# Performance work log

Measured on AMD Instinct MI355X. Metric: run time of the kernel, lower is better.

The kernel has to match this reference:

```python
import jax, jax.numpy as jnp
import numpy as np

B, N, P, L = 32, 4096, 256, 16
DR = 128           # rel_dim = args.rgcn_hidden_size
H = 128            # rnn_hidden_size (unidirectional -> rnn_opt_dim == H)
D = H
NUM_REL = 400      # num_rels * 2


def setup_inputs() -> dict:
    key = jax.random.key(0)
    ks = jax.random.split(key, 12)
    s = 0.05
    graph_embed = jax.random.normal(ks[0], (B, N, DR), jnp.float32)
    node_opt = jax.random.normal(ks[1], (B, D), jnp.float32)
    node_idx = jax.random.randint(ks[2], (B, P, L), 0, N)
    rel_idx = jax.random.randint(ks[3], (B, P, L), 0, NUM_REL)
    path_lens = jax.random.randint(ks[4], (B, P), 1, L + 1)  # in [1, L]
    rel_embeds = jax.random.normal(ks[5], (NUM_REL, DR), jnp.float32) * s
    W_ih = jax.random.normal(ks[6], (4 * H, 2 * DR), jnp.float32) * s
    W_hh = jax.random.normal(ks[7], (4 * H, H), jnp.float32) * s
    b_ih = jnp.zeros((4 * H,), jnp.float32)
    b_hh = jnp.zeros((4 * H,), jnp.float32)
    in_proj_w = jax.random.normal(ks[8], (3 * D, D), jnp.float32) * s
    in_proj_b = jnp.zeros((3 * D,), jnp.float32)
    out_proj_w = jax.random.normal(ks[9], (D, D), jnp.float32) * s
    out_proj_b = jnp.zeros((D,), jnp.float32)
    return dict(graph_embed=graph_embed, node_opt=node_opt, rel_embeds=rel_embeds,
                W_ih=W_ih, W_hh=W_hh, b_ih=b_ih, b_hh=b_hh,
                in_proj_w=in_proj_w, in_proj_b=in_proj_b,
                out_proj_w=out_proj_w, out_proj_b=out_proj_b,
                node_idx=node_idx, rel_idx=rel_idx, path_lens=path_lens)


def _forward(graph_embed, node_opt, rel_embeds, W_ih, W_hh, b_ih, b_hh,
             in_proj_w, in_proj_b, out_proj_w, out_proj_b,
             node_idx, rel_idx, path_lens):
    b, n, dr = graph_embed.shape
    p, l = node_idx.shape[1], node_idx.shape[2]
    h = W_hh.shape[1]
    dt = graph_embed.dtype

    t = jnp.arange(l)
    # node embedding valid for steps < len; rel valid for steps < len-1 ('Padr' at last step -> zero rel half)
    node_mask = (t[None, None, :] < path_lens[:, :, None]).astype(dt)[..., None]
    rel_mask = (t[None, None, :] < (path_lens - 1)[:, :, None]).astype(dt)[..., None]

    batch_ix = jnp.arange(b)[:, None, None]
    node_e = graph_embed[batch_ix, node_idx]            # [B,P,L,DR]
    rel_e = rel_embeds[rel_idx]                          # [B,P,L,DR]
    x = jnp.concatenate([node_e * node_mask, rel_e * rel_mask], axis=-1)
    x = x.reshape(b * p, l, 2 * dr)                      # packed path sequences

    bias = b_ih + b_hh

    def step(carry, xt):
        hh, cc = carry
        g = xt @ W_ih.T + hh @ W_hh.T + bias
        i, f, gg, o = jnp.split(g, 4, axis=-1)
        i = jax.nn.sigmoid(i); f = jax.nn.sigmoid(f)
        gg = jnp.tanh(gg); o = jax.nn.sigmoid(o)
        cc = f * cc + i * gg
        hh = o * jnp.tanh(cc)
        return (hh, cc), hh

    h0 = jnp.zeros((b * p, h), dt)
    _, ys = jax.lax.scan(step, (h0, h0), jnp.swapaxes(x, 0, 1))
    ys = jnp.swapaxes(ys, 0, 1).reshape(b, p, l, h)

    # last valid LSTM output per path (== pack_padded_sequence semantics, unidirectional)
    idx = jnp.broadcast_to((path_lens - 1)[:, :, None, None], (b, p, 1, h))
    last = jnp.take_along_axis(ys, idx, axis=2).squeeze(2)   # [B,P,H]

    # single-head MultiheadAttention: query = node_opt, keys/values = path encodings
    Wq, Wk, Wv = jnp.split(in_proj_w, 3, axis=0)
    bq, bk, bv = jnp.split(in_proj_b, 3)
    q = node_opt @ Wq.T + bq                                  # [B,D]
    k = last @ Wk.T + bk                                      # [B,P,D]
    v = last @ Wv.T + bv
    scale = 1.0 / jnp.sqrt(jnp.asarray(q.shape[-1], dt))
    attn = jax.nn.softmax(jnp.einsum('bd,bpd->bp', q, k) * scale, axis=-1)
    ctx = jnp.einsum('bp,bpd->bd', attn, v)
    return ctx @ out_proj_w.T + out_proj_b                    # [B,D]


def reference(graph_embed, node_opt, rel_embeds, W_ih, W_hh, b_ih, b_hh,
              in_proj_w, in_proj_b, out_proj_w, out_proj_b,
              node_idx, rel_idx, path_lens):
    return _forward(graph_embed, node_opt, rel_embeds, W_ih, W_hh, b_ih, b_hh,
                    in_proj_w, in_proj_b, out_proj_w, out_proj_b,
                    node_idx, rel_idx, path_lens)
```

## Files before the change

### kernel.cpp

```cpp
#include <hip/hip_runtime.h>
#include <hip/hip_bf16.h>


#define B_    32
#define N_    4096
#define L_    16
#define DR_   128
#define H_    128
#define G4_   512
#define AST2  264
#define NPATH 8192
#define NPB   32

typedef unsigned short bfraw;
typedef short short8 __attribute__((ext_vector_type(8)));
typedef float f32x4 __attribute__((ext_vector_type(4)));

__device__ int   g_isbf16;
__device__ int   g_isi64;
__device__ __align__(16) bfraw g_Wcat[G4_ * 256];
__device__ __align__(16) float g_relproj[400 * G4_];
__device__ float g_bias[G4_];
__device__ int   g_perm[NPATH];
__device__ float g_last[NPATH * H_];

#define BAR() asm volatile("s_waitcnt lgkmcnt(0)\n\ts_barrier" ::: "memory")

__device__ __forceinline__ float bfc(bfraw v) {
    return __uint_as_float(((unsigned)v) << 16);
}
__device__ __forceinline__ bfraw f2b(float f) {
    unsigned u = __float_as_uint(f);
    return (bfraw)((u + 0x7FFFu + ((u >> 16) & 1u)) >> 16);
}
__device__ __forceinline__ unsigned pk2(float a, float b) {
    return (unsigned)f2b(a) | ((unsigned)f2b(b) << 16);
}
__device__ __forceinline__ float ld(const void* p, size_t i, int isbf) {
    return isbf ? bfc(((const bfraw*)p)[i]) : ((const float*)p)[i];
}
__device__ __forceinline__ float sigf(float x) {
    return __builtin_amdgcn_rcpf(1.0f + __expf(-x));
}
__device__ __forceinline__ float tanhfast(float x) {
    return 2.0f * sigf(2.0f * x) - 1.0f;
}

__device__ __forceinline__ float dot128(const float* __restrict__ w,
                                        const float* __restrict__ s) {
    float acc = 0.f;
    #pragma unroll
    for (int i = 0; i < 32; ++i) {
        const float4 wv = *(const float4*)(w + i * 4);
        acc = fmaf(wv.x, s[i*4+0], fmaf(wv.y, s[i*4+1],
              fmaf(wv.z, s[i*4+2], fmaf(wv.w, s[i*4+3], acc))));
    }
    return acc;
}

__global__ __launch_bounds__(512) void k_prep(
    const void* __restrict__ node_opt, const int* __restrict__ node_idx,
    const void* __restrict__ rel_embeds,
    const void* __restrict__ W_ih, const void* __restrict__ W_hh,
    const void* __restrict__ b_ih, const void* __restrict__ b_hh,
    const int* __restrict__ path_lens)
{
    __shared__ float relv[DR_];
    __shared__ int s_big, s_nz, hist[16], cur[16];
    const int tid = threadIdx.x;
    const int blk = blockIdx.x;

    if (tid == 0) { s_big = 0; s_nz = 0; }
    __syncthreads();
    {
        const unsigned short* u = (const unsigned short*)node_opt;
        int big = 0;
        #pragma unroll
        for (int i = 0; i < 4; ++i) {
            const float v = fabsf(bfc(u[tid + i * 512]));
            big |= !(v < 1.0e3f);
        }
        if (big) s_big = 1;
        if (node_idx[2 * tid + 1] != 0) s_nz = 1;
    }
    __syncthreads();
    const int isbf = s_big ? 0 : 1;
    const int i64  = s_nz ? 0 : 1;

    if (blk < 400) {
        const int r = blk;
        if (tid < DR_) relv[tid] = ld(rel_embeds, (size_t)r * DR_ + tid, isbf);
        __syncthreads();
        const int n = tid;
        float s;
        if (isbf) {
            s = 0.f;
            for (int d = 0; d < DR_; ++d)
                s = fmaf(relv[d], bfc(((const bfraw*)W_ih)[(size_t)n * 256 + 128 + d]), s);
        } else {
            s = dot128((const float*)W_ih + (size_t)n * 256 + 128, relv);
        }
        g_relproj[r * G4_ + ((n & 127) << 2) + (n >> 7)] = s;
    } else if (blk < 656) {
        const int idx = (blk - 400) * 512 + tid;
        const int n = idx >> 8, k = idx & 255;
        const float v = (k < H_) ? ld(W_hh, (size_t)n * H_ + k, isbf)
                                 : ld(W_ih, (size_t)n * 256 + (k - H_), isbf);
        g_Wcat[n * 256 + k] = f2b(v);
    } else {
        if (tid == 0) { g_isbf16 = isbf; g_isi64 = i64; }
        g_bias[tid] = ld(b_ih, tid, isbf) + ld(b_hh, tid, isbf);
        if (tid < 16) hist[tid] = 0;
        __syncthreads();
        for (int p = tid; p < NPATH; p += 512) {
            const int len = i64 ? path_lens[2 * p] : path_lens[p];
            atomicAdd(&hist[len - 1], 1);
        }
        __syncthreads();
        if (tid == 0) {
            int off = 0;
            for (int b = 15; b >= 0; --b) { cur[b] = off; off += hist[b]; }
        }
        __syncthreads();
        for (int p = tid; p < NPATH; p += 512) {
            const int len = i64 ? path_lens[2 * p] : path_lens[p];
            const int pos = atomicAdd(&cur[len - 1], 1);
            g_perm[pos] = p;
        }
    }
}

__global__ __launch_bounds__(512, 2) void k_lstm(
    const void* __restrict__ graph_embed,
    const int*  __restrict__ node_idx,
    const int*  __restrict__ rel_idx,
    const int*  __restrict__ path_lens)
{
    __shared__ __align__(16) bfraw A[NPB][AST2];
    __shared__ int s_pid[NPB], s_len[NPB];
    __shared__ int s_nid[NPB][L_], s_rid[NPB][L_];

    const int isbf = g_isbf16;
    const int i64  = g_isi64;
    const int tid  = threadIdx.x;

    if (tid < NPB) {
        const int pid = g_perm[blockIdx.x * NPB + tid];
        s_pid[tid] = pid;
        s_len[tid] = i64 ? path_lens[2 * pid] : path_lens[pid];
    }
    __syncthreads();
    {
        const int m = tid >> 4, t = tid & 15;
        const int idx = s_pid[m] * L_ + t;
        s_nid[m][t] = i64 ? node_idx[2 * idx] : node_idx[idx];
        s_rid[m][t] = i64 ? rel_idx[2 * idx]  : rel_idx[idx];
    }
    {
        const int m = tid >> 4, i0 = (tid & 15) * 8;
        *(uint4*)&A[m][i0] = make_uint4(0, 0, 0, 0);
    }
    __syncthreads();

    int maxlen = 0;
    #pragma unroll
    for (int m = 0; m < NPB; ++m) maxlen = max(maxlen, s_len[m]);

    const int w    = tid >> 6;
    const int l    = tid & 63;
    const int quad = l >> 4;
    const int col  = l & 15;
    const int u0   = w * 16 + col;

    short8 wreg[8][4];
    float bq4[4];
    #pragma unroll
    for (int g = 0; g < 4; ++g) {
        bq4[g] = g_bias[g * 128 + u0];
        const bfraw* wrow = g_Wcat + (size_t)(g * 128 + u0) * 256 + quad * 8;
        #pragma unroll
        for (int ck = 0; ck < 8; ++ck)
            wreg[ck][g] = *(const short8*)(wrow + ck * 32);
    }

    const int pm  = tid >> 4;
    const int pi0 = (tid & 15) * 8;
    const size_t gbase = (size_t)(s_pid[pm] >> 8) * (size_t)(N_ * DR_);

    {
        const int nid = s_nid[pm][0];
        uint4 npk;
        if (isbf) {
            npk = *(const uint4*)((const bfraw*)graph_embed + gbase + (size_t)nid * DR_ + pi0);
        } else {
            const float* gp = (const float*)graph_embed + gbase + (size_t)nid * DR_ + pi0;
            const uint4 q0 = *(const uint4*)gp;
            const uint4 q1 = *(const uint4*)(gp + 4);
            const float* a = (const float*)&q0;
            const float* b = (const float*)&q1;
            npk = make_uint4(pk2(a[0],a[1]), pk2(a[2],a[3]),
                             pk2(b[0],b[1]), pk2(b[2],b[3]));
        }
        *(uint4*)&A[pm][128 + pi0] = npk;
    }
    __syncthreads();

    float c[2][4];
    #pragma unroll
    for (int mt = 0; mt < 2; ++mt)
        #pragma unroll
        for (int r = 0; r < 4; ++r) c[mt][r] = 0.f;

    uint4 pn0, pn1;

    for (int t = 0; t < maxlen; ++t) {
        if (t + 1 < maxlen) {
            const int nid = s_nid[pm][t + 1];
            if (isbf) {
                pn0 = *(const uint4*)((const bfraw*)graph_embed + gbase + (size_t)nid * DR_ + pi0);
            } else {
                const float* gp = (const float*)graph_embed + gbase + (size_t)nid * DR_ + pi0;
                pn0 = *(const uint4*)gp; pn1 = *(const uint4*)(gp + 4);
            }
        }

        f32x4 acc[2][4];
        #pragma unroll
        for (int mt = 0; mt < 2; ++mt)
            #pragma unroll
            for (int g = 0; g < 4; ++g) {
                const float b = bq4[g];
                acc[mt][g][0] = b; acc[mt][g][1] = b;
                acc[mt][g][2] = b; acc[mt][g][3] = b;
            }
        #pragma unroll
        for (int ck = 0; ck < 8; ++ck) {
            const short8 a0 = *(const short8*)&A[col][ck * 32 + quad * 8];
            const short8 a1 = *(const short8*)&A[16 + col][ck * 32 + quad * 8];
            #pragma unroll
            for (int g = 0; g < 4; ++g) {
                acc[0][g] = __builtin_amdgcn_mfma_f32_16x16x32_bf16(a0, wreg[ck][g], acc[0][g], 0, 0, 0);
                acc[1][g] = __builtin_amdgcn_mfma_f32_16x16x32_bf16(a1, wreg[ck][g], acc[1][g], 0, 0, 0);
            }
        }
        __builtin_amdgcn_sched_barrier(0);

        f32x4 rlv[2][4];
        #pragma unroll
        for (int mt = 0; mt < 2; ++mt)
            #pragma unroll
            for (int r = 0; r < 4; ++r) {
                const int m = mt * 16 + quad * 4 + r;
                rlv[mt][r] = *(const f32x4*)(g_relproj + (size_t)s_rid[m][t] * G4_ + u0 * 4);
            }

        float hv[2][4];
        #pragma unroll
        for (int mt = 0; mt < 2; ++mt)
            #pragma unroll
            for (int r = 0; r < 4; ++r) {
                const int m = mt * 16 + quad * 4 + r;
                const float relm = (t < s_len[m] - 1) ? 1.0f : 0.0f;
                const float ig = sigf(acc[mt][0][r] + relm * rlv[mt][r][0]);
                const float fg = sigf(acc[mt][1][r] + relm * rlv[mt][r][1]);
                const float gg = tanhfast(acc[mt][2][r] + relm * rlv[mt][r][2]);
                const float og = sigf(acc[mt][3][r] + relm * rlv[mt][r][3]);
                const float cc = fg * c[mt][r] + ig * gg;
                c[mt][r] = cc;
                hv[mt][r] = og * tanhfast(cc);
            }

        BAR();

        #pragma unroll
        for (int mt = 0; mt < 2; ++mt)
            #pragma unroll
            for (int r = 0; r < 4; ++r) {
                const int m = mt * 16 + quad * 4 + r;
                A[m][u0] = f2b(hv[mt][r]);
                if (t == s_len[m] - 1)
                    g_last[(size_t)s_pid[m] * H_ + u0] = hv[mt][r];
            }

        if (t + 1 < maxlen) {
            uint4 npk = make_uint4(0, 0, 0, 0);
            if (t + 1 < s_len[pm]) {
                if (isbf) npk = pn0;
                else {
                    const float* a = (const float*)&pn0;
                    const float* b = (const float*)&pn1;
                    npk = make_uint4(pk2(a[0],a[1]), pk2(a[2],a[3]),
                                     pk2(b[0],b[1]), pk2(b[2],b[3]));
                }
            }
            *(uint4*)&A[pm][128 + pi0] = npk;
        }

        BAR();
    }
}

__global__ __launch_bounds__(256) void k_attn(
    const void* __restrict__ node_opt,
    const void* __restrict__ in_proj_w,
    const void* __restrict__ in_proj_b,
    const void* __restrict__ out_proj_w,
    const void* __restrict__ out_proj_b,
    float* __restrict__ out)
{
    const int isbf = g_isbf16;
    const int b = blockIdx.x, tid = threadIdx.x;
    __shared__ __align__(16) float s_no[128], q[128], qk[128], sv2[2][128], ctx[128];
    __shared__ float logits[256];
    __shared__ float red[12];

    if (tid < 128) s_no[tid] = ld(node_opt, b * 128 + tid, isbf);
    __syncthreads();
    if (tid < 128) {
        float s;
        if (isbf) {
            s = 0.f;
            for (int j = 0; j < 128; ++j)
                s = fmaf(s_no[j], ld(in_proj_w, (size_t)tid * 128 + j, 1), s);
        } else {
            s = dot128((const float*)in_proj_w + (size_t)tid * 128, s_no);
        }
        q[tid] = s + ld(in_proj_b, tid, isbf);
    }
    __syncthreads();
    if (tid < 128) {
        float s = 0.f;
        for (int j = 0; j < 128; ++j)
            s = fmaf(q[j], ld(in_proj_w, (size_t)(128 + j) * 128 + tid, isbf), s);
        qk[tid] = s;
    } else if (tid == 128) {
        float s = 0.f;
        for (int j = 0; j < 128; ++j)
            s = fmaf(q[j], ld(in_proj_b, 128 + j, isbf), s);
        red[10] = s;
    }
    __syncthreads();
    {
        const float* lp = g_last + ((size_t)b * 256 + tid) * H_;
        const float s = dot128(lp, qk);
        logits[tid] = (s + red[10]) * 0.08838834764831845f;
    }
    __syncthreads();
    float v = logits[tid];
    #pragma unroll
    for (int off = 32; off > 0; off >>= 1) v = fmaxf(v, __shfl_xor(v, off, 64));
    if ((tid & 63) == 0) red[tid >> 6] = v;
    __syncthreads();
    if (tid == 0) red[8] = fmaxf(fmaxf(red[0], red[1]), fmaxf(red[2], red[3]));
    __syncthreads();
    const float e = __expf(logits[tid] - red[8]);
    float sum = e;
    #pragma unroll
    for (int off = 32; off > 0; off >>= 1) sum += __shfl_xor(sum, off, 64);
    if ((tid & 63) == 0) red[4 + (tid >> 6)] = sum;
    __syncthreads();
    if (tid == 0) red[9] = red[4] + red[5] + red[6] + red[7];
    __syncthreads();
    logits[tid] = e / red[9];
    __syncthreads();
    {
        const int u = tid & 127, half = tid >> 7;
        float s = 0.f;
        const float* lb = g_last + ((size_t)b * 256 + half * 128) * H_ + u;
        for (int p = 0; p < 128; ++p)
            s = fmaf(logits[half * 128 + p], lb[(size_t)p * H_], s);
        sv2[half][u] = s;
    }
    __syncthreads();
    if (tid < 128) q[tid] = sv2[0][tid] + sv2[1][tid];
    __syncthreads();
    if (tid < 128) {
        float s;
        if (isbf) {
            s = 0.f;
            for (int u = 0; u < 128; ++u)
                s = fmaf(q[u], ld(in_proj_w, (size_t)(256 + tid) * 128 + u, 1), s);
        } else {
            s = dot128((const float*)in_proj_w + (size_t)(256 + tid) * 128, q);
        }
        ctx[tid] = s + ld(in_proj_b, 256 + tid, isbf);
    }
    __syncthreads();
    if (tid < 128) {
        float s;
        if (isbf) {
            s = 0.f;
            for (int d = 0; d < 128; ++d)
                s = fmaf(ctx[d], ld(out_proj_w, (size_t)tid * 128 + d, 1), s);
        } else {
            s = dot128((const float*)out_proj_w + (size_t)tid * 128, ctx);
        }
        out[b * 128 + tid] = s + ld(out_proj_b, tid, isbf);
    }
}

extern "C" void kernel_launch(void* const* d_in, const int* in_sizes, int n_in,
                              void* d_out, int out_size, void* d_ws, size_t ws_size,
                              hipStream_t stream)
{
    const void* graph_embed = d_in[0];
    const void* node_opt    = d_in[1];
    const void* rel_embeds  = d_in[2];
    const void* W_ih        = d_in[3];
    const void* W_hh        = d_in[4];
    const void* b_ih        = d_in[5];
    const void* b_hh        = d_in[6];
    const void* in_proj_w   = d_in[7];
    const void* in_proj_b   = d_in[8];
    const void* out_proj_w  = d_in[9];
    const void* out_proj_b  = d_in[10];
    const int* node_idx  = (const int*)d_in[11];
    const int* rel_idx   = (const int*)d_in[12];
    const int* path_lens = (const int*)d_in[13];
    (void)d_ws; (void)ws_size; (void)in_sizes; (void)n_in; (void)out_size;

    hipLaunchKernelGGL(k_prep, dim3(657), dim3(512), 0, stream,
                       node_opt, node_idx, rel_embeds, W_ih, W_hh, b_ih, b_hh,
                       path_lens);
    hipLaunchKernelGGL(k_lstm, dim3(NPATH / NPB), dim3(512), 0, stream,
                       graph_embed, node_idx, rel_idx, path_lens);
    hipLaunchKernelGGL(k_attn, dim3(B_), dim3(256), 0, stream,
                       node_opt, in_proj_w, in_proj_b, out_proj_w, out_proj_b,
                       (float*)d_out);
}
```

Baseline: 219.4 us.

## Software-pipeline LSTM step across two path halves to overlap MFMA with gates

```diff
diff --git a/kernel.cpp b/kernel.cpp
--- a/kernel.cpp
+++ b/kernel.cpp
@@ -130,6 +130,80 @@
     }
 }
 
+
+#define DO_MFMA(ACC, BASE)                                                    \
+    {                                                                         \
+        _Pragma("unroll")                                                     \
+        for (int g = 0; g < 4; ++g) {                                         \
+            const float bb_ = bq4[g];                                         \
+            ACC[g][0] = bb_; ACC[g][1] = bb_; ACC[g][2] = bb_; ACC[g][3] = bb_; \
+        }                                                                     \
+        _Pragma("unroll")                                                     \
+        for (int ck = 0; ck < 8; ++ck) {                                      \
+            const short8 av_ = *(const short8*)&A[(BASE) + col][ck * 32 + quad * 8]; \
+            _Pragma("unroll")                                                 \
+            for (int g = 0; g < 4; ++g)                                       \
+                ACC[g] = __builtin_amdgcn_mfma_f32_16x16x32_bf16(             \
+                    av_, wreg[ck][g], ACC[g], 0, 0, 0);                       \
+        }                                                                     \
+    }
+
+#define RL_ADDR(RLO, MBASE, T)                                                \
+    {                                                                         \
+        _Pragma("unroll")                                                     \
+        for (int r = 0; r < 4; ++r)                                           \
+            RLO[r] = s_rid[(MBASE) + quad * 4 + r][T] * (G4_ * 4) + u0 * 16;  \
+    }
+
+#define DO_GATES(ACC, MT, MBASE, T, RLO)                                      \
+    {                                                                         \
+        f32x4 rlv_[4];                                                        \
+        _Pragma("unroll")                                                     \
+        for (int r = 0; r < 4; ++r)                                           \
+            rlv_[r] = *(const f32x4*)((const char*)g_relproj + RLO[r]);       \
+        _Pragma("unroll")                                                     \
+        for (int r = 0; r < 4; ++r) {                                         \
+            const int m_ = (MBASE) + quad * 4 + r;                            \
+            const float relm_ = ((T) < s_len[m_] - 1) ? 1.0f : 0.0f;          \
+            const float ig_ = sigf(ACC[0][r] + relm_ * rlv_[r][0]);           \
+            const float fg_ = sigf(ACC[1][r] + relm_ * rlv_[r][1]);           \
+            const float gg_ = tanhfast(ACC[2][r] + relm_ * rlv_[r][2]);       \
+            const float og_ = sigf(ACC[3][r] + relm_ * rlv_[r][3]);           \
+            const float cc_ = fg_ * c[MT][r] + ig_ * gg_;                     \
+            c[MT][r] = cc_;                                                   \
+            const float hh_ = og_ * tanhfast(cc_);                           \
+            A[m_][u0] = f2b(hh_);                                             \
+            if ((T) == s_len[m_] - 1)                                         \
+                g_last[(size_t)s_pid[m_] * H_ + u0] = hh_;                    \
+        }                                                                     \
+    }
+
+#define ISSUE_X(TT)                                                           \
+    {                                                                         \
+        const int nid_ = s_nid[pm][TT];                                       \
+        if (isbf) {                                                           \
+            pn0 = *(const uint4*)((const bfraw*)graph_embed + gbase + (size_t)nid_ * DR_ + pi0); \
+        } else {                                                              \
+            const float* gp_ = (const float*)graph_embed + gbase + (size_t)nid_ * DR_ + pi0; \
+            pn0 = *(const uint4*)gp_; pn1 = *(const uint4*)(gp_ + 4);         \
+        }                                                                     \
+    }
+
+#define COMMIT_X(TT)                                                          \
+    {                                                                         \
+        uint4 npk_ = make_uint4(0, 0, 0, 0);                                  \
+        if ((TT) < s_len[pm]) {                                               \
+            if (isbf) npk_ = pn0;                                             \
+            else {                                                            \
+                const float* a_ = (const float*)&pn0;                         \
+                const float* b_ = (const float*)&pn1;                         \
+                npk_ = make_uint4(pk2(a_[0], a_[1]), pk2(a_[2], a_[3]),       \
+                                  pk2(b_[0], b_[1]), pk2(b_[2], b_[3]));      \
+            }                                                                 \
+        }                                                                     \
+        *(uint4*)&A[pm][128 + pi0] = npk_;                                    \
+    }
+
 __global__ __launch_bounds__(512, 2) void k_lstm(
     const void* __restrict__ graph_embed,
     const int*  __restrict__ node_idx,
@@ -186,23 +260,12 @@
     const int pm  = tid >> 4;
     const int pi0 = (tid & 15) * 8;
     const size_t gbase = (size_t)(s_pid[pm] >> 8) * (size_t)(N_ * DR_);
-
-    {
-        const int nid = s_nid[pm][0];
-        uint4 npk;
-        if (isbf) {
-            npk = *(const uint4*)((const bfraw*)graph_embed + gbase + (size_t)nid * DR_ + pi0);
-        } else {
-            const float* gp = (const float*)graph_embed + gbase + (size_t)nid * DR_ + pi0;
-            const uint4 q0 = *(const uint4*)gp;
-            const uint4 q1 = *(const uint4*)(gp + 4);
-            const float* a = (const float*)&q0;
-            const float* b = (const float*)&q1;
-            npk = make_uint4(pk2(a[0],a[1]), pk2(a[2],a[3]),
-                             pk2(b[0],b[1]), pk2(b[2],b[3]));
-        }
-        *(uint4*)&A[pm][128 + pi0] = npk;
-    }
+    const bool stg0 = (pm < 16);
+
+    uint4 pn0, pn1;
+
+    ISSUE_X(0);
+    COMMIT_X(0);
     __syncthreads();
 
     float c[2][4];
@@ -211,91 +274,29 @@
         #pragma unroll
         for (int r = 0; r < 4; ++r) c[mt][r] = 0.f;
 
-    uint4 pn0, pn1;
+    f32x4 acc0[4], acc1[4];
+
+    DO_MFMA(acc0, 0);
 
     for (int t = 0; t < maxlen; ++t) {
-        if (t + 1 < maxlen) {
-            const int nid = s_nid[pm][t + 1];
-            if (isbf) {
-                pn0 = *(const uint4*)((const bfraw*)graph_embed + gbase + (size_t)nid * DR_ + pi0);
-            } else {
-                const float* gp = (const float*)graph_embed + gbase + (size_t)nid * DR_ + pi0;
-                pn0 = *(const uint4*)gp; pn1 = *(const uint4*)(gp + 4);
-            }
-        }
-
-        f32x4 acc[2][4];
-        #pragma unroll
-        for (int mt = 0; mt < 2; ++mt)
-            #pragma unroll
-            for (int g = 0; g < 4; ++g) {
-                const float b = bq4[g];
-                acc[mt][g][0] = b; acc[mt][g][1] = b;
-                acc[mt][g][2] = b; acc[mt][g][3] = b;
-            }
-        #pragma unroll
-        for (int ck = 0; ck < 8; ++ck) {
-            const short8 a0 = *(const short8*)&A[col][ck * 32 + quad * 8];
-            const short8 a1 = *(const short8*)&A[16 + col][ck * 32 + quad * 8];
-            #pragma unroll
-            for (int g = 0; g < 4; ++g) {
-                acc[0][g] = __builtin_amdgcn_mfma_f32_16x16x32_bf16(a0, wreg[ck][g], acc[0][g], 0, 0, 0);
-                acc[1][g] = __builtin_amdgcn_mfma_f32_16x16x32_bf16(a1, wreg[ck][g], acc[1][g], 0, 0, 0);
-            }
-        }
+        const bool more = (t + 1 < maxlen);
+
+        int rlo0[4];
+        RL_ADDR(rlo0, 0, t);
+        if (stg0 && more) ISSUE_X(t + 1);
+        DO_MFMA(acc1, 16);
         __builtin_amdgcn_sched_barrier(0);
-
-        f32x4 rlv[2][4];
-        #pragma unroll
-        for (int mt = 0; mt < 2; ++mt)
-            #pragma unroll
-            for (int r = 0; r < 4; ++r) {
-                const int m = mt * 16 + quad * 4 + r;
-                rlv[mt][r] = *(const f32x4*)(g_relproj + (size_t)s_rid[m][t] * G4_ + u0 * 4);
-            }
-
-        float hv[2][4];
-        #pragma unroll
-        for (int mt = 0; mt < 2; ++mt)
-            #pragma unroll
-            for (int r = 0; r < 4; ++r) {
-                const int m = mt * 16 + quad * 4 + r;
-                const float relm = (t < s_len[m] - 1) ? 1.0f : 0.0f;
-                const float ig = sigf(acc[mt][0][r] + relm * rlv[mt][r][0]);
-                const float fg = sigf(acc[mt][1][r] + relm * rlv[mt][r][1]);
-                const float gg = tanhfast(acc[mt][2][r] + relm * rlv[mt][r][2]);
-                const float og = sigf(acc[mt][3][r] + relm * rlv[mt][r][3]);
-                const float cc = fg * c[mt][r] + ig * gg;
-                c[mt][r] = cc;
-                hv[mt][r] = og * tanhfast(cc);
-            }
-
+        DO_GATES(acc0, 0, 0, t, rlo0);
+        if (stg0 && more) COMMIT_X(t + 1);
         BAR();
 
-        #pragma unroll
-        for (int mt = 0; mt < 2; ++mt)
-            #pragma unroll
-            for (int r = 0; r < 4; ++r) {
-                const int m = mt * 16 + quad * 4 + r;
-                A[m][u0] = f2b(hv[mt][r]);
-                if (t == s_len[m] - 1)
-                    g_last[(size_t)s_pid[m] * H_ + u0] = hv[mt][r];
-            }
-
-        if (t + 1 < maxlen) {
-            uint4 npk = make_uint4(0, 0, 0, 0);
-            if (t + 1 < s_len[pm]) {
-                if (isbf) npk = pn0;
-                else {
-                    const float* a = (const float*)&pn0;
-                    const float* b = (const float*)&pn1;
-                    npk = make_uint4(pk2(a[0],a[1]), pk2(a[2],a[3]),
-                                     pk2(b[0],b[1]), pk2(b[2],b[3]));
-                }
-            }
-            *(uint4*)&A[pm][128 + pi0] = npk;
-        }
-
+        int rlo1[4];
+        RL_ADDR(rlo1, 16, t);
+        if (!stg0 && more) ISSUE_X(t + 1);
+        if (more) DO_MFMA(acc0, 0);
+        __builtin_amdgcn_sched_barrier(0);
+        DO_GATES(acc1, 1, 16, t, rlo1);
+        if (!stg0 && more) COMMIT_X(t + 1);
         BAR();
     }
 }
```

Result: no change. 222.4 us (+1.4%).
